# Performance work log

Measured on AMD Instinct MI355X. Metric: run time of the kernel, lower is better.

The kernel has to match this reference:

```python
import jax, jax.numpy as jnp
import numpy as np

B, LONG, SHORT, D, NH, HD = 512, 1000, 50, 64, 4, 16
NUM_ITEMS, TOPK = 100000, 50
NBUCKETS, HASHL, HASHD = 1024, 4, 16  # NOTE: 4 hash layers of D//4 so concat matches item_dim (source default 3 is a shape bug)


def lin(x, w, b):
    return x @ w.T + b


def ln(x, g, b):
    m = x.mean(-1, keepdims=True)
    v = ((x - m) ** 2).mean(-1, keepdims=True)
    return (x - m) / jnp.sqrt(v + 1e-5) * g + b


def setup_inputs() -> dict:
    key = jax.random.key(0)
    ks = jax.random.split(key, 24)
    rn = lambda i, s: jax.random.normal(ks[i], s, jnp.float32) * 0.02
    emb = rn(0, (NUM_ITEMS + 1, D)).at[0].set(0.0)  # padding_idx=0 row zeroed
    return dict(
        user_features=jax.random.normal(ks[1], (B, D), jnp.float32),
        target_item_id=jax.random.randint(ks[2], (B,), 0, NUM_ITEMS + 1),
        short_hist_ids=jax.random.randint(ks[3], (B, SHORT), 0, NUM_ITEMS + 1),
        long_hist_ids=jax.random.randint(ks[4], (B, LONG), 0, NUM_ITEMS + 1),
        item_emb=emb,
        tproj_w=rn(5, (D, D)), tproj_b=jnp.zeros((D,), jnp.float32),
        attn_w1=rn(6, (64, 3 * D)), attn_b1=jnp.zeros((64,), jnp.float32),
        attn_w2=rn(7, (1, 64)), attn_b2=jnp.zeros((1,), jnp.float32),
        hash_emb=rn(8, (HASHL, NBUCKETS, HASHD)),
        sdim_w=rn(9, (D, D)), sdim_b=jnp.zeros((D,), jnp.float32),
        tf_qkv_w=rn(10, (2, 3 * D, D)), tf_qkv_b=jnp.zeros((2, 3 * D), jnp.float32),
        tf_out_w=rn(11, (2, D, D)), tf_out_b=jnp.zeros((2, D), jnp.float32),
        tf_ln1_g=jnp.ones((2, D), jnp.float32), tf_ln1_b=jnp.zeros((2, D), jnp.float32),
        tf_ff1_w=rn(12, (2, 2 * D, D)), tf_ff1_b=jnp.zeros((2, 2 * D), jnp.float32),
        tf_ff2_w=rn(13, (2, D, 2 * D)), tf_ff2_b=jnp.zeros((2, D), jnp.float32),
        tf_ln2_g=jnp.ones((2, D), jnp.float32), tf_ln2_b=jnp.zeros((2, D), jnp.float32),
        fus_w1=rn(14, (256, 4 * D)), fus_b1=jnp.zeros((256,), jnp.float32),
        fus_w2=rn(15, (128, 256)), fus_b2=jnp.zeros((128,), jnp.float32),
        fus_w3=rn(16, (1, 128)), fus_b3=jnp.zeros((1,), jnp.float32),
    )


def sim_forward(user_features, item_emb, tproj_w, tproj_b, attn_w1, attn_b1,
                attn_w2, attn_b2, hash_emb, sdim_w, sdim_b, tf_qkv_w, tf_qkv_b,
                tf_out_w, tf_out_b, tf_ln1_g, tf_ln1_b, tf_ff1_w, tf_ff1_b,
                tf_ff2_w, tf_ff2_b, tf_ln2_g, tf_ln2_b, fus_w1, fus_b1, fus_w2,
                fus_b2, fus_w3, fus_b3, target_item_id, short_hist_ids, long_hist_ids):
    # target projection
    target_emb = lin(item_emb[target_item_id], tproj_w, tproj_b)         # [B,D]
    # ---- hard search over long history ----
    long_emb = item_emb[long_hist_ids]                                    # [B,L,D]
    t = jnp.broadcast_to(target_emb[:, None, :], long_emb.shape)
    cc = jnp.concatenate([t, long_emb, long_emb * t], axis=-1)            # [B,L,3D]
    scores = lin(jax.nn.relu(lin(cc, attn_w1, attn_b1)), attn_w2, attn_b2)[..., 0]
    attn = jax.nn.softmax(scores, axis=-1)                                # [B,L]
    top_w, top_i = jax.lax.top_k(attn, TOPK)
    top_w = jax.nn.softmax(top_w, axis=-1)
    top_e = jnp.take_along_axis(long_emb, top_i[..., None], axis=1)       # [B,K,D]
    hard_repr = (top_w[..., None] * top_e).sum(axis=1)                    # [B,D]
    # ---- SDIM soft search ----
    bucket = long_hist_ids % NBUCKETS
    h = hash_emb[:, bucket].mean(axis=2)                                  # [HL,B,HD]
    hash_repr = jnp.moveaxis(h, 0, 1).reshape(h.shape[1], HASHL * HASHD)  # [B,D]
    soft_repr = lin(hash_repr + long_emb.mean(axis=1), sdim_w, sdim_b)    # [B,D]
    # ---- BST transformer over short history (post-norm, relu, dropout=eval) ----
    x = item_emb[short_hist_ids]                                          # [B,S,D]
    for l in range(2):
        qkv = lin(x, tf_qkv_w[l], tf_qkv_b[l])
        q, k, v = jnp.split(qkv, 3, axis=-1)
        q = q.reshape(B, SHORT, NH, HD); k = k.reshape(B, SHORT, NH, HD); v = v.reshape(B, SHORT, NH, HD)
        sc = jnp.einsum('bqhd,bkhd->bhqk', q, k) / np.sqrt(HD).astype(np.float32)
        a = jax.nn.softmax(sc, axis=-1)
        o = jnp.einsum('bhqk,bkhd->bqhd', a, v).reshape(B, SHORT, D)
        x = ln(x + lin(o, tf_out_w[l], tf_out_b[l]), tf_ln1_g[l], tf_ln1_b[l])
        f = lin(jax.nn.relu(lin(x, tf_ff1_w[l], tf_ff1_b[l])), tf_ff2_w[l], tf_ff2_b[l])
        x = ln(x + f, tf_ln2_g[l], tf_ln2_b[l])
    bst_repr = x.mean(axis=1)                                             # [B,D]
    # ---- fusion MLP ----
    combined = jnp.concatenate([user_features, hard_repr, soft_repr, bst_repr], axis=-1)
    hdn = jax.nn.relu(lin(combined, fus_w1, fus_b1))
    hdn = jax.nn.relu(lin(hdn, fus_w2, fus_b2))
    return lin(hdn, fus_w3, fus_b3)[..., 0]                               # [B]


def reference(user_features, target_item_id, short_hist_ids, long_hist_ids,
              item_emb, tproj_w, tproj_b, attn_w1, attn_b1, attn_w2, attn_b2,
              hash_emb, sdim_w, sdim_b, tf_qkv_w, tf_qkv_b, tf_out_w, tf_out_b,
              tf_ln1_g, tf_ln1_b, tf_ff1_w, tf_ff1_b, tf_ff2_w, tf_ff2_b,
              tf_ln2_g, tf_ln2_b, fus_w1, fus_b1, fus_w2, fus_b2, fus_w3, fus_b3):
    return sim_forward(user_features, item_emb, tproj_w, tproj_b, attn_w1, attn_b1,
                       attn_w2, attn_b2, hash_emb, sdim_w, sdim_b, tf_qkv_w, tf_qkv_b,
                       tf_out_w, tf_out_b, tf_ln1_g, tf_ln1_b, tf_ff1_w, tf_ff1_b,
                       tf_ff2_w, tf_ff2_b, tf_ln2_g, tf_ln2_b, fus_w1, fus_b1,
                       fus_w2, fus_b2, fus_w3, fus_b3, target_item_id,
                       short_hist_ids, long_hist_ids)
```

## Files before the change

### kernel.cpp

```cpp
#include <hip/hip_runtime.h>
#include <math.h>

#define NB 512
#define LONGN 1000
#define SHORTN 50
#define TOPKN 50
#define HALFN 500
#define NG 8
#define EROW 72
#define BROW 72
#define F1ROW 136

typedef __attribute__((ext_vector_type(8))) short bf16x8;
typedef __attribute__((ext_vector_type(4))) float f32x4;

__device__ __forceinline__ float dot4(float4 a, float4 b) {
  return a.x*b.x + a.y*b.y + a.z*b.z + a.w*b.w;
}

template<int N>
__device__ __forceinline__ float dotN(const float* w, const float* x) {
  const float4* w4 = (const float4*)w;
  const float4* x4 = (const float4*)x;
  float a0 = 0.f, a1 = 0.f, a2 = 0.f, a3 = 0.f;
  #pragma unroll
  for (int k = 0; k < N/4; k += 4) {
    a0 += dot4(w4[k],   x4[k]);
    a1 += dot4(w4[k+1], x4[k+1]);
    a2 += dot4(w4[k+2], x4[k+2]);
    a3 += dot4(w4[k+3], x4[k+3]);
  }
  return (a0 + a1) + (a2 + a3);
}

__device__ __forceinline__ float wave_sum(float v) {
  #pragma unroll
  for (int off = 32; off > 0; off >>= 1) v += __shfl_xor(v, off);
  return v;
}
__device__ __forceinline__ float wave_max(float v) {
  #pragma unroll
  for (int off = 32; off > 0; off >>= 1) v = fmaxf(v, __shfl_xor(v, off));
  return v;
}

__device__ __forceinline__ unsigned short f2bf(float x) {
  unsigned u = __float_as_uint(x);
  return (unsigned short)((u + 0x7fffu + ((u >> 16) & 1u)) >> 16);
}

__global__ __launch_bounds__(256, 4) void hard_scores_kernel(
    const int* __restrict__ target_item_id,
    const int* __restrict__ long_hist_ids,
    const float* __restrict__ item_emb,
    const float* __restrict__ tproj_w, const float* __restrict__ tproj_b,
    const float* __restrict__ attn_w1, const float* __restrict__ attn_b1,
    const float* __restrict__ attn_w2, const float* __restrict__ attn_b2,
    const float* __restrict__ hash_emb,
    float* __restrict__ scores_ws, float* __restrict__ partA,
    float* __restrict__ partH)
{
  __shared__ __align__(16) short Abf[64*EROW];
  __shared__ __align__(16) short Ebuf[2][64*EROW];
  __shared__ __align__(16) float tv[64];
  __shared__ __align__(16) float te[64];
  __shared__ __align__(16) float2 cw[64];
  __shared__ int idsL[HALFN];
  __shared__ __align__(16) float redE[4*64];

  const int bid = blockIdx.x;
  const int b = bid >> 1, half = bid & 1;
  const int base = half * HALFN;
  const int tid = threadIdx.x;
  const int wid = tid >> 6, lane = tid & 63;

  if (tid < 64) tv[tid] = item_emb[target_item_id[b]*64 + tid];
  for (int l = tid; l < HALFN; l += 256) idsL[l] = long_hist_ids[b*LONGN + base + l];
  __syncthreads();
  if (tid < 64) te[tid] = tproj_b[tid] + dotN<64>(tproj_w + tid*64, tv);
  __syncthreads();
  if (tid < 64) {
    float c = attn_b1[tid] + dotN<64>(attn_w1 + tid*192, te);
    cw[tid] = make_float2(c, attn_w2[tid]);
  }
  for (int idx = tid; idx < 4096; idx += 256) {
    int i = idx >> 6, j = idx & 63;
    Abf[i*EROW + j] = (short)f2bf(attn_w1[i*192 + 64 + j] + attn_w1[i*192 + 128 + j]*te[j]);
  }
  __syncthreads();

  bf16x8 a00,a01,a10,a11,a20,a21,a30,a31;
  {
    const short* ap = Abf + (lane & 15)*EROW + ((lane >> 4) << 3);
    a00 = *(const bf16x8*)(ap +  0*EROW);  a01 = *(const bf16x8*)(ap +  0*EROW + 32);
    a10 = *(const bf16x8*)(ap + 16*EROW);  a11 = *(const bf16x8*)(ap + 16*EROW + 32);
    a20 = *(const bf16x8*)(ap + 32*EROW);  a21 = *(const bf16x8*)(ap + 32*EROW + 32);
    a30 = *(const bf16x8*)(ap + 48*EROW);  a31 = *(const bf16x8*)(ap + 48*EROW + 32);
  }

  const float b2s = attn_b2[0];
  const int it_g = tid >> 2;
  const int dimg = (tid & 3) * 16;

  float4 sE0 = {0,0,0,0}, sE1 = {0,0,0,0}, sE2 = {0,0,0,0}, sE3 = {0,0,0,0};

  {
    const float4* ep = (const float4*)(item_emb + (size_t)idsL[it_g]*64 + dimg);
    float4 r0 = ep[0], r1 = ep[1], r2 = ep[2], r3 = ep[3];
    sE0.x+=r0.x; sE0.y+=r0.y; sE0.z+=r0.z; sE0.w+=r0.w;
    sE1.x+=r1.x; sE1.y+=r1.y; sE1.z+=r1.z; sE1.w+=r1.w;
    sE2.x+=r2.x; sE2.y+=r2.y; sE2.z+=r2.z; sE2.w+=r2.w;
    sE3.x+=r3.x; sE3.y+=r3.y; sE3.z+=r3.z; sE3.w+=r3.w;
    bf16x8 w0, w1;
    w0[0]=(short)f2bf(r0.x); w0[1]=(short)f2bf(r0.y); w0[2]=(short)f2bf(r0.z); w0[3]=(short)f2bf(r0.w);
    w0[4]=(short)f2bf(r1.x); w0[5]=(short)f2bf(r1.y); w0[6]=(short)f2bf(r1.z); w0[7]=(short)f2bf(r1.w);
    w1[0]=(short)f2bf(r2.x); w1[1]=(short)f2bf(r2.y); w1[2]=(short)f2bf(r2.z); w1[3]=(short)f2bf(r2.w);
    w1[4]=(short)f2bf(r3.x); w1[5]=(short)f2bf(r3.y); w1[6]=(short)f2bf(r3.z); w1[7]=(short)f2bf(r3.w);
    short* dst = &Ebuf[0][it_g*EROW + dimg];
    *(bf16x8*)dst = w0;  *(bf16x8*)(dst + 8) = w1;
  }
  __syncthreads();

  int buf = 0;
  for (int g = 0; g < NG; ++g) {
    float4 r0={0,0,0,0}, r1={0,0,0,0}, r2={0,0,0,0}, r3={0,0,0,0};
    const bool more = (g + 1 < NG);
    if (more) {
      const int gi = (g+1)*64 + it_g;
      if (gi < HALFN) {
        const float4* ep = (const float4*)(item_emb + (size_t)idsL[gi]*64 + dimg);
        r0 = ep[0]; r1 = ep[1]; r2 = ep[2]; r3 = ep[3];
      }
    }

    f32x4 acc0={0,0,0,0}, acc1={0,0,0,0}, acc2={0,0,0,0}, acc3={0,0,0,0};
    {
      const short* ep = &Ebuf[buf][(wid*16 + (lane & 15))*EROW + ((lane >> 4) << 3)];
      bf16x8 b0 = *(const bf16x8*)(ep);
      bf16x8 b1 = *(const bf16x8*)(ep + 32);
      acc0 = __builtin_amdgcn_mfma_f32_16x16x32_bf16(a00, b0, acc0, 0, 0, 0);
      acc0 = __builtin_amdgcn_mfma_f32_16x16x32_bf16(a01, b1, acc0, 0, 0, 0);
      acc1 = __builtin_amdgcn_mfma_f32_16x16x32_bf16(a10, b0, acc1, 0, 0, 0);
      acc1 = __builtin_amdgcn_mfma_f32_16x16x32_bf16(a11, b1, acc1, 0, 0, 0);
      acc2 = __builtin_amdgcn_mfma_f32_16x16x32_bf16(a20, b0, acc2, 0, 0, 0);
      acc2 = __builtin_amdgcn_mfma_f32_16x16x32_bf16(a21, b1, acc2, 0, 0, 0);
      acc3 = __builtin_amdgcn_mfma_f32_16x16x32_bf16(a30, b0, acc3, 0, 0, 0);
      acc3 = __builtin_amdgcn_mfma_f32_16x16x32_bf16(a31, b1, acc3, 0, 0, 0);
    }
    float p = 0.f;
    {
      const int rbase = (lane >> 4) << 2;
      #pragma unroll
      for (int r = 0; r < 4; ++r) {
        float2 c0 = cw[ 0 + rbase + r];
        float2 c1 = cw[16 + rbase + r];
        float2 c2 = cw[32 + rbase + r];
        float2 c3 = cw[48 + rbase + r];
        p += c0.y * fmaxf(acc0[r] + c0.x, 0.f);
        p += c1.y * fmaxf(acc1[r] + c1.x, 0.f);
        p += c2.y * fmaxf(acc2[r] + c2.x, 0.f);
        p += c3.y * fmaxf(acc3[r] + c3.x, 0.f);
      }
    }
    p += __shfl_xor(p, 16);
    p += __shfl_xor(p, 32);
    if (lane < 16) {
      const int gi = g*64 + wid*16 + lane;
      if (gi < HALFN) scores_ws[b*LONGN + base + gi] = b2s + p;
    }

    if (more) {
      sE0.x+=r0.x; sE0.y+=r0.y; sE0.z+=r0.z; sE0.w+=r0.w;
      sE1.x+=r1.x; sE1.y+=r1.y; sE1.z+=r1.z; sE1.w+=r1.w;
      sE2.x+=r2.x; sE2.y+=r2.y; sE2.z+=r2.z; sE2.w+=r2.w;
      sE3.x+=r3.x; sE3.y+=r3.y; sE3.z+=r3.z; sE3.w+=r3.w;
      bf16x8 w0, w1;
      w0[0]=(short)f2bf(r0.x); w0[1]=(short)f2bf(r0.y); w0[2]=(short)f2bf(r0.z); w0[3]=(short)f2bf(r0.w);
      w0[4]=(short)f2bf(r1.x); w0[5]=(short)f2bf(r1.y); w0[6]=(short)f2bf(r1.z); w0[7]=(short)f2bf(r1.w);
      w1[0]=(short)f2bf(r2.x); w1[1]=(short)f2bf(r2.y); w1[2]=(short)f2bf(r2.z); w1[3]=(short)f2bf(r2.w);
      w1[4]=(short)f2bf(r3.x); w1[5]=(short)f2bf(r3.y); w1[6]=(short)f2bf(r3.z); w1[7]=(short)f2bf(r3.w);
      short* dst = &Ebuf[buf ^ 1][it_g*EROW + dimg];
      *(bf16x8*)dst = w0;  *(bf16x8*)(dst + 8) = w1;
    }
    __syncthreads();
    buf ^= 1;
  }

  {
    float* red = (float*)&Ebuf[0][0];
    const int b17 = tid * 17;
    red[b17+ 0]=sE0.x; red[b17+ 1]=sE0.y; red[b17+ 2]=sE0.z; red[b17+ 3]=sE0.w;
    red[b17+ 4]=sE1.x; red[b17+ 5]=sE1.y; red[b17+ 6]=sE1.z; red[b17+ 7]=sE1.w;
    red[b17+ 8]=sE2.x; red[b17+ 9]=sE2.y; red[b17+10]=sE2.z; red[b17+11]=sE2.w;
    red[b17+12]=sE3.x; red[b17+13]=sE3.y; red[b17+14]=sE3.z; red[b17+15]=sE3.w;
    __syncthreads();
    if (tid < 64) {
      const int dg = tid >> 4, dw = tid & 15;
      float s = 0.f;
      for (int j = 0; j < 64; ++j) s += red[(j*4 + dg)*17 + dw];
      partA[bid*64 + tid] = s;
    }
  }

  {
    const int hl = lane >> 4, dd = lane & 15;
    const float* hb = hash_emb + hl*1024*16 + dd;
    float accH = 0.f;
    for (int l = wid; l < HALFN; l += 4)
      accH += hb[(idsL[l] & 1023)*16];
    redE[wid*64 + lane] = accH;
  }
  __syncthreads();
  if (wid == 0)
    partH[bid*64 + lane] = redE[lane] + redE[64+lane] + redE[128+lane] + redE[192+lane];
}

__global__ __launch_bounds__(256) void bst_prep_kernel(
    const float* __restrict__ qkv_w, const float* __restrict__ out_w,
    const float* __restrict__ ff1_w, const float* __restrict__ ff2_w,
    short* __restrict__ wF)
{
  const int t = blockIdx.x*256 + threadIdx.x;
  if (t >= 8192) return;
  const int fid = t >> 6, lane = t & 63;
  const int n16 = lane & 15, k8 = (lane >> 4) * 8;
  const float* src;
  if (fid < 48)      { int f=fid,    l=f/24, r=f%24, nt=r>>1, kc=r&1;
    src = qkv_w + l*12288 + (nt*16+n16)*64 + kc*32 + k8; }
  else if (fid < 64) { int f=fid-48, l=f>>3, r=f&7,  nt=r>>1, kc=r&1;
    src = out_w + l*4096 + (nt*16+n16)*64 + kc*32 + k8; }
  else if (fid < 96) { int f=fid-64, l=f>>4, r=f&15, nt=r>>1, kc=r&1;
    src = ff1_w + l*8192 + (nt*16+n16)*64 + kc*32 + k8; }
  else               { int f=fid-96, l=f>>4, r=f&15, nt=r>>2, kc=r&3;
    src = ff2_w + l*8192 + (nt*16+n16)*128 + kc*32 + k8; }
  short* dst = wF + fid*512 + lane*8;
  #pragma unroll
  for (int j = 0; j < 8; ++j) dst[j] = (short)f2bf(src[j]);
}

__global__ __launch_bounds__(512, 2) void bst_kernel(
    const int* __restrict__ short_ids, const float* __restrict__ item_emb,
    const short* __restrict__ wF,
    const float* __restrict__ qkv_b, const float* __restrict__ out_b,
    const float* __restrict__ ln1_g, const float* __restrict__ ln1_b,
    const float* __restrict__ ff1_b, const float* __restrict__ ff2_b,
    const float* __restrict__ ln2_g, const float* __restrict__ ln2_b,
    float* __restrict__ bst_out)
{
  __shared__ __align__(16) float xf[SHORTN*64];
  __shared__ __align__(16) short xbf[64*BROW];
  __shared__ __align__(16) float qf[SHORTN*68];
  __shared__ __align__(16) float arena[SHORTN*132];
  __shared__ __align__(16) short obf[64*BROW];

  short* f1bf = (short*)arena;

  const int b = blockIdx.x, tid = threadIdx.x;
  const int w8 = tid >> 6, lane = tid & 63;
  const int mh = w8 & 1, wg = w8 >> 1;
  const int n16 = lane & 15;
  const int kg8 = (lane >> 4) << 3;
  const int mrow = (lane >> 4) << 2;
  const int rb = 32*mh;

  for (int idx = tid; idx < SHORTN*64; idx += 512) {
    int s = idx >> 6, j = idx & 63;
    float v = item_emb[short_ids[b*SHORTN + s]*64 + j];
    xf[idx] = v;
    xbf[s*BROW + j] = (short)f2bf(v);
  }
  for (int idx = tid; idx < 14*BROW; idx += 512) {
    xbf[50*BROW + idx] = 0;
    obf[50*BROW + idx] = 0;
  }
  __syncthreads();

  for (int l = 0; l < 2; ++l) {
    {
      const short* ap = xbf + (rb + n16)*BROW + kg8;
      bf16x8 A00 = *(const bf16x8*)(ap);            bf16x8 A01 = *(const bf16x8*)(ap + 32);
      bf16x8 A10 = *(const bf16x8*)(ap + 16*BROW);  bf16x8 A11 = *(const bf16x8*)(ap + 16*BROW + 32);
      #pragma unroll
      for (int t = 0; t < 3; ++t) {
        const int nt = wg*3 + t;
        const short* bp = wF + (size_t)(l*24 + nt*2)*512 + lane*8;
        bf16x8 B0 = *(const bf16x8*)(bp);
        bf16x8 B1 = *(const bf16x8*)(bp + 512);
        f32x4 c0={0,0,0,0}, c1={0,0,0,0};
        c0 = __builtin_amdgcn_mfma_f32_16x16x32_bf16(A00, B0, c0, 0,0,0);
        c0 = __builtin_amdgcn_mfma_f32_16x16x32_bf16(A01, B1, c0, 0,0,0);
        c1 = __builtin_amdgcn_mfma_f32_16x16x32_bf16(A10, B0, c1, 0,0,0);
        c1 = __builtin_amdgcn_mfma_f32_16x16x32_bf16(A11, B1, c1, 0,0,0);
        const int c = nt*16 + n16;
        const float bias = qkv_b[l*192 + c];
        #pragma unroll
        for (int r = 0; r < 4; ++r) {
          const int r0 = rb + mrow + r;
          const int r1 = r0 + 16;
          float v0 = c0[r] + bias;
          float v1 = c1[r] + bias;
          if (c < 64) {
            qf[r0*68 + c] = v0;
            if (r1 < SHORTN) qf[r1*68 + c] = v1;
          } else {
            const int cc = c - 64;
            arena[r0*132 + cc] = v0;
            if (r1 < SHORTN) arena[r1*132 + cc] = v1;
          }
        }
      }
    }
    __syncthreads();

    if (tid < 8*SHORTN) {
      const int pair = tid >> 1, khalf = tid & 1;
      const int h = pair / SHORTN, s = pair - h*SHORTN;
      const float4* qp = (const float4*)(qf + s*68 + h*16);
      const float4 qA = qp[0], qB2 = qp[1], qC = qp[2], qD = qp[3];
      float ss = 0.f;
      float4 oa0 = {0,0,0,0}, oa1 = {0,0,0,0}, oa2 = {0,0,0,0}, oa3 = {0,0,0,0};
      const int t0 = khalf*25;
      for (int t2 = t0; t2 < t0 + 25; ++t2) {
        const float4* kp = (const float4*)(arena + t2*132 + h*16);
        float d = dot4(qA,kp[0]) + dot4(qB2,kp[1]) + dot4(qC,kp[2]) + dot4(qD,kp[3]);
        float p = __expf(d*0.25f);
        ss += p;
        const float4* vp = (const float4*)(arena + t2*132 + 64 + h*16);
        float4 v0 = vp[0], v1 = vp[1], v2 = vp[2], v3 = vp[3];
        oa0.x += p*v0.x; oa0.y += p*v0.y; oa0.z += p*v0.z; oa0.w += p*v0.w;
        oa1.x += p*v1.x; oa1.y += p*v1.y; oa1.z += p*v1.z; oa1.w += p*v1.w;
        oa2.x += p*v2.x; oa2.y += p*v2.y; oa2.z += p*v2.z; oa2.w += p*v2.w;
        oa3.x += p*v3.x; oa3.y += p*v3.y; oa3.z += p*v3.z; oa3.w += p*v3.w;
      }
      ss    += __shfl_xor(ss, 1);
      oa0.x += __shfl_xor(oa0.x, 1); oa0.y += __shfl_xor(oa0.y, 1);
      oa0.z += __shfl_xor(oa0.z, 1); oa0.w += __shfl_xor(oa0.w, 1);
      oa1.x += __shfl_xor(oa1.x, 1); oa1.y += __shfl_xor(oa1.y, 1);
      oa1.z += __shfl_xor(oa1.z, 1); oa1.w += __shfl_xor(oa1.w, 1);
      oa2.x += __shfl_xor(oa2.x, 1); oa2.y += __shfl_xor(oa2.y, 1);
      oa2.z += __shfl_xor(oa2.z, 1); oa2.w += __shfl_xor(oa2.w, 1);
      oa3.x += __shfl_xor(oa3.x, 1); oa3.y += __shfl_xor(oa3.y, 1);
      oa3.z += __shfl_xor(oa3.z, 1); oa3.w += __shfl_xor(oa3.w, 1);
      if (khalf == 0) {
        const float inv = 1.f/ss;
        bf16x8 w0, w1;
        w0[0]=(short)f2bf(oa0.x*inv); w0[1]=(short)f2bf(oa0.y*inv);
        w0[2]=(short)f2bf(oa0.z*inv); w0[3]=(short)f2bf(oa0.w*inv);
        w0[4]=(short)f2bf(oa1.x*inv); w0[5]=(short)f2bf(oa1.y*inv);
        w0[6]=(short)f2bf(oa1.z*inv); w0[7]=(short)f2bf(oa1.w*inv);
        w1[0]=(short)f2bf(oa2.x*inv); w1[1]=(short)f2bf(oa2.y*inv);
        w1[2]=(short)f2bf(oa2.z*inv); w1[3]=(short)f2bf(oa2.w*inv);
        w1[4]=(short)f2bf(oa3.x*inv); w1[5]=(short)f2bf(oa3.y*inv);
        w1[6]=(short)f2bf(oa3.z*inv); w1[7]=(short)f2bf(oa3.w*inv);
        short* op = obf + s*BROW + h*16;
        *(bf16x8*)op = w0;  *(bf16x8*)(op + 8) = w1;
      }
    }
    __syncthreads();

    {
      const short* ap = obf + (rb + n16)*BROW + kg8;
      bf16x8 A00 = *(const bf16x8*)(ap);            bf16x8 A01 = *(const bf16x8*)(ap + 32);
      bf16x8 A10 = *(const bf16x8*)(ap + 16*BROW);  bf16x8 A11 = *(const bf16x8*)(ap + 16*BROW + 32);
      const int nt = wg;
      const short* bp = wF + (size_t)(48 + l*8 + nt*2)*512 + lane*8;
      bf16x8 B0 = *(const bf16x8*)(bp);
      bf16x8 B1 = *(const bf16x8*)(bp + 512);
      f32x4 c0={0,0,0,0}, c1={0,0,0,0};
      c0 = __builtin_amdgcn_mfma_f32_16x16x32_bf16(A00, B0, c0, 0,0,0);
      c0 = __builtin_amdgcn_mfma_f32_16x16x32_bf16(A01, B1, c0, 0,0,0);
      c1 = __builtin_amdgcn_mfma_f32_16x16x32_bf16(A10, B0, c1, 0,0,0);
      c1 = __builtin_amdgcn_mfma_f32_16x16x32_bf16(A11, B1, c1, 0,0,0);
      const int c = nt*16 + n16;
      const float bias = out_b[l*64 + c];
      #pragma unroll
      for (int r = 0; r < 4; ++r) {
        const int r0 = rb + mrow + r;
        const int r1 = r0 + 16;
        arena[r0*68 + c] = xf[r0*64 + c] + bias + c0[r];
        if (r1 < SHORTN) arena[r1*68 + c] = xf[r1*64 + c] + bias + c1[r];
      }
      for (int idx = tid; idx < 14*F1ROW; idx += 512) f1bf[50*F1ROW + idx] = 0;
    }
    __syncthreads();

    {
      const float g = ln1_g[l*64 + lane], bb = ln1_b[l*64 + lane];
      for (int s = w8; s < SHORTN; s += 8) {
        float y = arena[s*68 + lane];
        float mean = wave_sum(y) * (1.f/64.f);
        float dv = y - mean;
        float var = wave_sum(dv*dv) * (1.f/64.f);
        float r = dv / sqrtf(var + 1e-5f) * g + bb;
        xf[s*64 + lane] = r;
        xbf[s*BROW + lane] = (short)f2bf(r);
      }
    }
    __syncthreads();

    {
      const short* ap = xbf + (rb + n16)*BROW + kg8;
      bf16x8 A00 = *(const bf16x8*)(ap);            bf16x8 A01 = *(const bf16x8*)(ap + 32);
      bf16x8 A10 = *(const bf16x8*)(ap + 16*BROW);  bf16x8 A11 = *(const bf16x8*)(ap + 16*BROW + 32);
      #pragma unroll
      for (int t = 0; t < 2; ++t) {
        const int nt = wg*2 + t;
        const short* bp = wF + (size_t)(64 + l*16 + nt*2)*512 + lane*8;
        bf16x8 B0 = *(const bf16x8*)(bp);
        bf16x8 B1 = *(const bf16x8*)(bp + 512);
        f32x4 c0={0,0,0,0}, c1={0,0,0,0};
        c0 = __builtin_amdgcn_mfma_f32_16x16x32_bf16(A00, B0, c0, 0,0,0);
        c0 = __builtin_amdgcn_mfma_f32_16x16x32_bf16(A01, B1, c0, 0,0,0);
        c1 = __builtin_amdgcn_mfma_f32_16x16x32_bf16(A10, B0, c1, 0,0,0);
        c1 = __builtin_amdgcn_mfma_f32_16x16x32_bf16(A11, B1, c1, 0,0,0);
        const int c = nt*16 + n16;
        const float bias = ff1_b[l*128 + c];
        #pragma unroll
        for (int r = 0; r < 4; ++r) {
          const int r0 = rb + mrow + r;
          const int r1 = r0 + 16;
          f1bf[r0*F1ROW + c] = (short)f2bf(fmaxf(c0[r] + bias, 0.f));
          if (r1 < SHORTN) f1bf[r1*F1ROW + c] = (short)f2bf(fmaxf(c1[r] + bias, 0.f));
        }
      }
    }
    __syncthreads();

    {
      const int nt = wg;
      f32x4 c0={0,0,0,0}, c1={0,0,0,0};
      #pragma unroll
      for (int kc = 0; kc < 4; ++kc) {
        const short* ap = f1bf + (rb + n16)*F1ROW + kc*32 + kg8;
        bf16x8 A0 = *(const bf16x8*)(ap);
        bf16x8 A1 = *(const bf16x8*)(ap + 16*F1ROW);
        const short* bp = wF + (size_t)(96 + l*16 + nt*4 + kc)*512 + lane*8;
        bf16x8 B = *(const bf16x8*)(bp);
        c0 = __builtin_amdgcn_mfma_f32_16x16x32_bf16(A0, B, c0, 0,0,0);
        c1 = __builtin_amdgcn_mfma_f32_16x16x32_bf16(A1, B, c1, 0,0,0);
      }
      __syncthreads();
      const int c = nt*16 + n16;
      const float bias = ff2_b[l*64 + c];
      #pragma unroll
      for (int r = 0; r < 4; ++r) {
        const int r0 = rb + mrow + r;
        const int r1 = r0 + 16;
        arena[r0*68 + c] = xf[r0*64 + c] + bias + c0[r];
        if (r1 < SHORTN) arena[r1*68 + c] = xf[r1*64 + c] + bias + c1[r];
      }
    }
    __syncthreads();

    {
      const float g = ln2_g[l*64 + lane], bb = ln2_b[l*64 + lane];
      for (int s = w8; s < SHORTN; s += 8) {
        float y = arena[s*68 + lane];
        float mean = wave_sum(y) * (1.f/64.f);
        float dv = y - mean;
        float var = wave_sum(dv*dv) * (1.f/64.f);
        float r = dv / sqrtf(var + 1e-5f) * g + bb;
        xf[s*64 + lane] = r;
        xbf[s*BROW + lane] = (short)f2bf(r);
      }
    }
    __syncthreads();
  }

  float acc = 0.f;
  for (int s = w8; s < SHORTN; s += 8) acc += xf[s*64 + lane];
  qf[w8*64 + lane] = acc;
  __syncthreads();
  if (w8 == 0) {
    float t = qf[lane];
    #pragma unroll
    for (int w = 1; w < 8; ++w) t += qf[w*64 + lane];
    bst_out[b*64 + lane] = t * (1.f/50.f);
  }
}

__global__ __launch_bounds__(512) void hard_finish_fusion_kernel(
    const int* __restrict__ long_hist_ids,
    const float* __restrict__ item_emb,
    const float* __restrict__ sdim_w, const float* __restrict__ sdim_b,
    const float* __restrict__ scores_ws,
    const float* __restrict__ partA, const float* __restrict__ partH,
    const float* __restrict__ user, const float* __restrict__ bst,
    const float* __restrict__ w1, const float* __restrict__ b1,
    const float* __restrict__ w2, const float* __restrict__ b2,
    const float* __restrict__ w3, const float* __restrict__ b3,
    float* __restrict__ out)
{
  __shared__ __align__(16) float scores[LONGN];
  __shared__ int   idsL[LONGN];
  __shared__ __align__(16) unsigned long long kv[1024];
  __shared__ __align__(16) float redE[8*64];
  __shared__ __align__(16) float vecbuf[64];
  __shared__ float redV[8];
  __shared__ float selV[TOPKN];
  __shared__ int   selI[TOPKN];
  __shared__ __align__(16) float comb[256];
  __shared__ __align__(16) float h1[256];
  __shared__ __align__(16) float h2[128];

  const int b = blockIdx.x;
  const int tid = threadIdx.x;
  const int wid = tid >> 6, lane = tid & 63;

  for (int l = tid; l < LONGN; l += 512) {
    scores[l] = scores_ws[b*LONGN + l];
    idsL[l] = long_hist_ids[b*LONGN + l];
  }
  if (tid < 64)                          comb[tid] = user[b*64 + tid];
  else if (tid >= 192 && tid < 256)      comb[tid] = bst[b*64 + tid - 192];
  __syncthreads();

  if (tid < 64)
    vecbuf[tid] = (partA[(2*b)*64 + tid] + partA[(2*b+1)*64 + tid]
                 + partH[(2*b)*64 + tid] + partH[(2*b+1)*64 + tid]) * (1.f/1000.f);
  __syncthreads();
  if (tid < 64)
    comb[128 + tid] = sdim_b[tid] + dotN<64>(sdim_w + tid*64, vecbuf);

  float mx = -INFINITY;
  for (int l = tid; l < LONGN; l += 512) mx = fmaxf(mx, scores[l]);
  mx = wave_max(mx);
  if (lane == 0) redV[wid] = mx;
  __syncthreads();
  mx = redV[0];
  #pragma unroll
  for (int w = 1; w < 8; ++w) mx = fmaxf(mx, redV[w]);
  __syncthreads();
  float sm = 0.f;
  for (int l = tid; l < LONGN; l += 512) {
    float a = expf(scores[l] - mx);
    scores[l] = a;
    sm += a;
  }
  sm = wave_sum(sm);
  if (lane == 0) redV[wid] = sm;
  __syncthreads();
  {
    float tot = redV[0];
    #pragma unroll
    for (int w = 1; w < 8; ++w) tot += redV[w];
    const float inv = 1.f / tot;
    for (int l = tid; l < LONGN; l += 512) scores[l] *= inv;
  }
  __syncthreads();

  for (int l = tid; l < 1024; l += 512) {
    if (l < LONGN) {
      unsigned vb = __float_as_uint(scores[l]);
      kv[l] = ((unsigned long long)(~vb) << 32) | (unsigned)l;
    } else {
      kv[l] = 0xFFFFFFFFFFFFFFFFull;
    }
  }
  __syncthreads();

  for (int k = 2; k <= 1024; k <<= 1) {
    for (int j = k >> 1; j > 0; j >>= 1) {
      {
        const int p = tid;
        const int i = ((p & ~(j-1)) << 1) | (p & (j-1));
        const int m = i + j;
        const bool up = ((i & k) == 0);
        unsigned long long a = kv[i], c = kv[m];
        if ((a > c) == up) { kv[i] = c; kv[m] = a; }
      }
      __syncthreads();
    }
  }

  if (tid < TOPKN) {
    unsigned long long key = kv[tid];
    selI[tid] = (int)(unsigned)(key & 0xFFFFFFFFu);
    selV[tid] = __uint_as_float(~(unsigned)(key >> 32));
  }
  __syncthreads();

  if (wid == 0) {
    float v = (lane < TOPKN) ? selV[lane] : -INFINITY;
    float m2 = wave_max(v);
    float e = (lane < TOPKN) ? expf(v - m2) : 0.f;
    float s2 = wave_sum(e);
    if (lane < TOPKN) selV[lane] = e / s2;
  }
  __syncthreads();

  float accR = 0.f;
  for (int r = wid; r < TOPKN; r += 8)
    accR += selV[r] * item_emb[idsL[selI[r]]*64 + lane];
  redE[wid*64 + lane] = accR;
  __syncthreads();
  if (wid == 0) {
    float t = redE[lane];
    #pragma unroll
    for (int w = 1; w < 8; ++w) t += redE[w*64 + lane];
    comb[64 + lane] = t;
  }
  __syncthreads();

  if (tid < 256) h1[tid] = fmaxf(b1[tid] + dotN<256>(w1 + tid*256, comb), 0.f);
  __syncthreads();
  if (tid < 128) h2[tid] = fmaxf(b2[tid] + dotN<256>(w2 + tid*256, h1), 0.f);
  __syncthreads();
  if (tid < 64) {
    float p = w3[tid]*h2[tid] + w3[tid+64]*h2[tid+64];
    p = wave_sum(p);
    if (tid == 0) out[b] = p + b3[0];
  }
}

extern "C" void kernel_launch(void* const* d_in, const int* in_sizes, int n_in,
                              void* d_out, int out_size, void* d_ws, size_t ws_size,
                              hipStream_t stream) {
  const float* user_features  = (const float*)d_in[0];
  const int*   target_item_id = (const int*)  d_in[1];
  const int*   short_hist_ids = (const int*)  d_in[2];
  const int*   long_hist_ids  = (const int*)  d_in[3];
  const float* item_emb       = (const float*)d_in[4];
  const float* tproj_w  = (const float*)d_in[5];
  const float* tproj_b  = (const float*)d_in[6];
  const float* attn_w1  = (const float*)d_in[7];
  const float* attn_b1  = (const float*)d_in[8];
  const float* attn_w2  = (const float*)d_in[9];
  const float* attn_b2  = (const float*)d_in[10];
  const float* hash_emb = (const float*)d_in[11];
  const float* sdim_w   = (const float*)d_in[12];
  const float* sdim_b   = (const float*)d_in[13];
  const float* tf_qkv_w = (const float*)d_in[14];
  const float* tf_qkv_b = (const float*)d_in[15];
  const float* tf_out_w = (const float*)d_in[16];
  const float* tf_out_b = (const float*)d_in[17];
  const float* tf_ln1_g = (const float*)d_in[18];
  const float* tf_ln1_b = (const float*)d_in[19];
  const float* tf_ff1_w = (const float*)d_in[20];
  const float* tf_ff1_b = (const float*)d_in[21];
  const float* tf_ff2_w = (const float*)d_in[22];
  const float* tf_ff2_b = (const float*)d_in[23];
  const float* tf_ln2_g = (const float*)d_in[24];
  const float* tf_ln2_b = (const float*)d_in[25];
  const float* fus_w1   = (const float*)d_in[26];
  const float* fus_b1   = (const float*)d_in[27];
  const float* fus_w2   = (const float*)d_in[28];
  const float* fus_b2   = (const float*)d_in[29];
  const float* fus_w3   = (const float*)d_in[30];
  const float* fus_b3   = (const float*)d_in[31];

  float* ws = (float*)d_ws;
  float* hard = ws;
  float* soft = hard + NB*64;
  float* bst  = soft + NB*64;
  float* scores_ws = bst + NB*64;
  float* partA = scores_ws + NB*LONGN;
  float* partH = partA + NB*2*64;
  short* wF    = (short*)(partH + NB*2*64);

  bst_prep_kernel<<<32, 256, 0, stream>>>(tf_qkv_w, tf_out_w, tf_ff1_w, tf_ff2_w, wF);
  hard_scores_kernel<<<2*NB, 256, 0, stream>>>(target_item_id, long_hist_ids,
      item_emb, tproj_w, tproj_b, attn_w1, attn_b1, attn_w2, attn_b2,
      hash_emb, scores_ws, partA, partH);
  bst_kernel<<<NB, 512, 0, stream>>>(short_hist_ids, item_emb, wF,
      tf_qkv_b, tf_out_b, tf_ln1_g, tf_ln1_b, tf_ff1_b, tf_ff2_b,
      tf_ln2_g, tf_ln2_b, bst);
  hard_finish_fusion_kernel<<<NB, 512, 0, stream>>>(long_hist_ids, item_emb,
      sdim_w, sdim_b, scores_ws, partA, partH,
      user_features, bst, fus_w1, fus_b1, fus_w2, fus_b2, fus_w3, fus_b3,
      (float*)d_out);
}
```

Before: 141.5 us.

## Fold BST weight prep into hard_scores and deepen gather prefetch to two groups

```diff
diff --git a/kernel.cpp b/kernel.cpp
--- a/kernel.cpp
+++ b/kernel.cpp
@@ -49,7 +49,7 @@
   return (unsigned short)((u + 0x7fffu + ((u >> 16) & 1u)) >> 16);
 }
 
-__global__ __launch_bounds__(256, 4) void hard_scores_kernel(
+__global__ __launch_bounds__(256, 3) void hard_scores_kernel(
     const int* __restrict__ target_item_id,
     const int* __restrict__ long_hist_ids,
     const float* __restrict__ item_emb,
@@ -57,6 +57,9 @@
     const float* __restrict__ attn_w1, const float* __restrict__ attn_b1,
     const float* __restrict__ attn_w2, const float* __restrict__ attn_b2,
     const float* __restrict__ hash_emb,
+    const float* __restrict__ qkv_w, const float* __restrict__ out_w,
+    const float* __restrict__ ff1_w, const float* __restrict__ ff2_w,
+    short* __restrict__ wF,
     float* __restrict__ scores_ws, float* __restrict__ partA,
     float* __restrict__ partH)
 {
@@ -74,6 +77,24 @@
   const int tid = threadIdx.x;
   const int wid = tid >> 6, lane = tid & 63;
 
+  if (bid < 32) {
+    const int t = bid*256 + tid;
+    const int fid = t >> 6, plane = t & 63;
+    const int n16p = plane & 15, k8 = (plane >> 4) * 8;
+    const float* src;
+    if (fid < 48)      { int f=fid,    l=f/24, r=f%24, nt=r>>1, kc=r&1;
+      src = qkv_w + l*12288 + (nt*16+n16p)*64 + kc*32 + k8; }
+    else if (fid < 64) { int f=fid-48, l=f>>3, r=f&7,  nt=r>>1, kc=r&1;
+      src = out_w + l*4096 + (nt*16+n16p)*64 + kc*32 + k8; }
+    else if (fid < 96) { int f=fid-64, l=f>>4, r=f&15, nt=r>>1, kc=r&1;
+      src = ff1_w + l*8192 + (nt*16+n16p)*64 + kc*32 + k8; }
+    else               { int f=fid-96, l=f>>4, r=f&15, nt=r>>2, kc=r&3;
+      src = ff2_w + l*8192 + (nt*16+n16p)*128 + kc*32 + k8; }
+    short* dst = wF + fid*512 + plane*8;
+    #pragma unroll
+    for (int j = 0; j < 8; ++j) dst[j] = (short)f2bf(src[j]);
+  }
+
   if (tid < 64) tv[tid] = item_emb[target_item_id[b]*64 + tid];
   for (int l = tid; l < HALFN; l += 256) idsL[l] = long_hist_ids[b*LONGN + base + l];
   __syncthreads();
@@ -103,88 +124,90 @@
   const int dimg = (tid & 3) * 16;
 
   float4 sE0 = {0,0,0,0}, sE1 = {0,0,0,0}, sE2 = {0,0,0,0}, sE3 = {0,0,0,0};
-
-  {
-    const float4* ep = (const float4*)(item_emb + (size_t)idsL[it_g]*64 + dimg);
-    float4 r0 = ep[0], r1 = ep[1], r2 = ep[2], r3 = ep[3];
-    sE0.x+=r0.x; sE0.y+=r0.y; sE0.z+=r0.z; sE0.w+=r0.w;
-    sE1.x+=r1.x; sE1.y+=r1.y; sE1.z+=r1.z; sE1.w+=r1.w;
-    sE2.x+=r2.x; sE2.y+=r2.y; sE2.z+=r2.z; sE2.w+=r2.w;
-    sE3.x+=r3.x; sE3.y+=r3.y; sE3.z+=r3.z; sE3.w+=r3.w;
-    bf16x8 w0, w1;
-    w0[0]=(short)f2bf(r0.x); w0[1]=(short)f2bf(r0.y); w0[2]=(short)f2bf(r0.z); w0[3]=(short)f2bf(r0.w);
-    w0[4]=(short)f2bf(r1.x); w0[5]=(short)f2bf(r1.y); w0[6]=(short)f2bf(r1.z); w0[7]=(short)f2bf(r1.w);
-    w1[0]=(short)f2bf(r2.x); w1[1]=(short)f2bf(r2.y); w1[2]=(short)f2bf(r2.z); w1[3]=(short)f2bf(r2.w);
-    w1[4]=(short)f2bf(r3.x); w1[5]=(short)f2bf(r3.y); w1[6]=(short)f2bf(r3.z); w1[7]=(short)f2bf(r3.w);
-    short* dst = &Ebuf[0][it_g*EROW + dimg];
-    *(bf16x8*)dst = w0;  *(bf16x8*)(dst + 8) = w1;
-  }
-  __syncthreads();
-
-  int buf = 0;
-  for (int g = 0; g < NG; ++g) {
-    float4 r0={0,0,0,0}, r1={0,0,0,0}, r2={0,0,0,0}, r3={0,0,0,0};
-    const bool more = (g + 1 < NG);
-    if (more) {
-      const int gi = (g+1)*64 + it_g;
-      if (gi < HALFN) {
-        const float4* ep = (const float4*)(item_emb + (size_t)idsL[gi]*64 + dimg);
-        r0 = ep[0]; r1 = ep[1]; r2 = ep[2]; r3 = ep[3];
-      }
-    }
-
-    f32x4 acc0={0,0,0,0}, acc1={0,0,0,0}, acc2={0,0,0,0}, acc3={0,0,0,0};
-    {
-      const short* ep = &Ebuf[buf][(wid*16 + (lane & 15))*EROW + ((lane >> 4) << 3)];
-      bf16x8 b0 = *(const bf16x8*)(ep);
-      bf16x8 b1 = *(const bf16x8*)(ep + 32);
-      acc0 = __builtin_amdgcn_mfma_f32_16x16x32_bf16(a00, b0, acc0, 0, 0, 0);
-      acc0 = __builtin_amdgcn_mfma_f32_16x16x32_bf16(a01, b1, acc0, 0, 0, 0);
-      acc1 = __builtin_amdgcn_mfma_f32_16x16x32_bf16(a10, b0, acc1, 0, 0, 0);
-      acc1 = __builtin_amdgcn_mfma_f32_16x16x32_bf16(a11, b1, acc1, 0, 0, 0);
-      acc2 = __builtin_amdgcn_mfma_f32_16x16x32_bf16(a20, b0, acc2, 0, 0, 0);
-      acc2 = __builtin_amdgcn_mfma_f32_16x16x32_bf16(a21, b1, acc2, 0, 0, 0);
-      acc3 = __builtin_amdgcn_mfma_f32_16x16x32_bf16(a30, b0, acc3, 0, 0, 0);
-      acc3 = __builtin_amdgcn_mfma_f32_16x16x32_bf16(a31, b1, acc3, 0, 0, 0);
-    }
-    float p = 0.f;
-    {
-      const int rbase = (lane >> 4) << 2;
-      #pragma unroll
-      for (int r = 0; r < 4; ++r) {
-        float2 c0 = cw[ 0 + rbase + r];
-        float2 c1 = cw[16 + rbase + r];
-        float2 c2 = cw[32 + rbase + r];
-        float2 c3 = cw[48 + rbase + r];
-        p += c0.y * fmaxf(acc0[r] + c0.x, 0.f);
-        p += c1.y * fmaxf(acc1[r] + c1.x, 0.f);
-        p += c2.y * fmaxf(acc2[r] + c2.x, 0.f);
-        p += c3.y * fmaxf(acc3[r] + c3.x, 0.f);
-      }
-    }
-    p += __shfl_xor(p, 16);
-    p += __shfl_xor(p, 32);
-    if (lane < 16) {
-      const int gi = g*64 + wid*16 + lane;
-      if (gi < HALFN) scores_ws[b*LONGN + base + gi] = b2s + p;
-    }
-
-    if (more) {
-      sE0.x+=r0.x; sE0.y+=r0.y; sE0.z+=r0.z; sE0.w+=r0.w;
-      sE1.x+=r1.x; sE1.y+=r1.y; sE1.z+=r1.z; sE1.w+=r1.w;
-      sE2.x+=r2.x; sE2.y+=r2.y; sE2.z+=r2.z; sE2.w+=r2.w;
-      sE3.x+=r3.x; sE3.y+=r3.y; sE3.z+=r3.z; sE3.w+=r3.w;
-      bf16x8 w0, w1;
-      w0[0]=(short)f2bf(r0.x); w0[1]=(short)f2bf(r0.y); w0[2]=(short)f2bf(r0.z); w0[3]=(short)f2bf(r0.w);
-      w0[4]=(short)f2bf(r1.x); w0[5]=(short)f2bf(r1.y); w0[6]=(short)f2bf(r1.z); w0[7]=(short)f2bf(r1.w);
-      w1[0]=(short)f2bf(r2.x); w1[1]=(short)f2bf(r2.y); w1[2]=(short)f2bf(r2.z); w1[3]=(short)f2bf(r2.w);
-      w1[4]=(short)f2bf(r3.x); w1[5]=(short)f2bf(r3.y); w1[6]=(short)f2bf(r3.z); w1[7]=(short)f2bf(r3.w);
-      short* dst = &Ebuf[buf ^ 1][it_g*EROW + dimg];
-      *(bf16x8*)dst = w0;  *(bf16x8*)(dst + 8) = w1;
-    }
-    __syncthreads();
-    buf ^= 1;
-  }
+  float4 pA0, pA1, pA2, pA3;
+  float4 pB0, pB1, pB2, pB3;
+
+#define LOADG(G, R0, R1, R2, R3)                                              \
+  {                                                                           \
+    R0 = make_float4(0,0,0,0); R1 = R0; R2 = R0; R3 = R0;                     \
+    const int gi_ = (G)*64 + it_g;                                            \
+    if (gi_ < HALFN) {                                                        \
+      const float4* ep_ = (const float4*)(item_emb + (size_t)idsL[gi_]*64 + dimg); \
+      R0 = ep_[0]; R1 = ep_[1]; R2 = ep_[2]; R3 = ep_[3];                     \
+    }                                                                         \
+  }
+
+#define STOREG(DST, R0, R1, R2, R3)                                           \
+  {                                                                           \
+    sE0.x+=R0.x; sE0.y+=R0.y; sE0.z+=R0.z; sE0.w+=R0.w;                       \
+    sE1.x+=R1.x; sE1.y+=R1.y; sE1.z+=R1.z; sE1.w+=R1.w;                       \
+    sE2.x+=R2.x; sE2.y+=R2.y; sE2.z+=R2.z; sE2.w+=R2.w;                       \
+    sE3.x+=R3.x; sE3.y+=R3.y; sE3.z+=R3.z; sE3.w+=R3.w;                       \
+    bf16x8 w0_, w1_;                                                          \
+    w0_[0]=(short)f2bf(R0.x); w0_[1]=(short)f2bf(R0.y);                       \
+    w0_[2]=(short)f2bf(R0.z); w0_[3]=(short)f2bf(R0.w);                       \
+    w0_[4]=(short)f2bf(R1.x); w0_[5]=(short)f2bf(R1.y);                       \
+    w0_[6]=(short)f2bf(R1.z); w0_[7]=(short)f2bf(R1.w);                       \
+    w1_[0]=(short)f2bf(R2.x); w1_[1]=(short)f2bf(R2.y);                       \
+    w1_[2]=(short)f2bf(R2.z); w1_[3]=(short)f2bf(R2.w);                       \
+    w1_[4]=(short)f2bf(R3.x); w1_[5]=(short)f2bf(R3.y);                       \
+    w1_[6]=(short)f2bf(R3.z); w1_[7]=(short)f2bf(R3.w);                       \
+    short* dst_ = &Ebuf[DST][it_g*EROW + dimg];                               \
+    *(bf16x8*)dst_ = w0_;  *(bf16x8*)(dst_ + 8) = w1_;                        \
+  }
+
+#define COMPUTEG(BUF, G)                                                      \
+  {                                                                           \
+    f32x4 acc0={0,0,0,0}, acc1={0,0,0,0}, acc2={0,0,0,0}, acc3={0,0,0,0};     \
+    const short* ep_ = &Ebuf[BUF][(wid*16 + (lane & 15))*EROW + ((lane >> 4) << 3)]; \
+    bf16x8 b0_ = *(const bf16x8*)(ep_);                                       \
+    bf16x8 b1_ = *(const bf16x8*)(ep_ + 32);                                  \
+    acc0 = __builtin_amdgcn_mfma_f32_16x16x32_bf16(a00, b0_, acc0, 0,0,0);    \
+    acc0 = __builtin_amdgcn_mfma_f32_16x16x32_bf16(a01, b1_, acc0, 0,0,0);    \
+    acc1 = __builtin_amdgcn_mfma_f32_16x16x32_bf16(a10, b0_, acc1, 0,0,0);    \
+    acc1 = __builtin_amdgcn_mfma_f32_16x16x32_bf16(a11, b1_, acc1, 0,0,0);    \
+    acc2 = __builtin_amdgcn_mfma_f32_16x16x32_bf16(a20, b0_, acc2, 0,0,0);    \
+    acc2 = __builtin_amdgcn_mfma_f32_16x16x32_bf16(a21, b1_, acc2, 0,0,0);    \
+    acc3 = __builtin_amdgcn_mfma_f32_16x16x32_bf16(a30, b0_, acc3, 0,0,0);    \
+    acc3 = __builtin_amdgcn_mfma_f32_16x16x32_bf16(a31, b1_, acc3, 0,0,0);    \
+    float p_ = 0.f;                                                           \
+    const int rbase_ = (lane >> 4) << 2;                                      \
+    _Pragma("unroll")                                                         \
+    for (int r = 0; r < 4; ++r) {                                             \
+      float2 c0_ = cw[ 0 + rbase_ + r];                                       \
+      float2 c1_ = cw[16 + rbase_ + r];                                       \
+      float2 c2_ = cw[32 + rbase_ + r];                                       \
+      float2 c3_ = cw[48 + rbase_ + r];                                       \
+      p_ += c0_.y * fmaxf(acc0[r] + c0_.x, 0.f);                              \
+      p_ += c1_.y * fmaxf(acc1[r] + c1_.x, 0.f);                              \
+      p_ += c2_.y * fmaxf(acc2[r] + c2_.x, 0.f);                              \
+      p_ += c3_.y * fmaxf(acc3[r] + c3_.x, 0.f);                              \
+    }                                                                         \
+    p_ += __shfl_xor(p_, 16);                                                 \
+    p_ += __shfl_xor(p_, 32);                                                 \
+    if (lane < 16) {                                                          \
+      const int gi_ = (G)*64 + wid*16 + lane;                                 \
+      if (gi_ < HALFN) scores_ws[b*LONGN + base + gi_] = b2s + p_;            \
+    }                                                                         \
+  }
+
+  LOADG(0, pA0, pA1, pA2, pA3);
+  LOADG(1, pB0, pB1, pB2, pB3);
+  STOREG(0, pA0, pA1, pA2, pA3);
+  __syncthreads();
+
+  LOADG(2, pA0, pA1, pA2, pA3);  COMPUTEG(0, 0);  STOREG(1, pB0, pB1, pB2, pB3);  __syncthreads();
+  LOADG(3, pB0, pB1, pB2, pB3);  COMPUTEG(1, 1);  STOREG(0, pA0, pA1, pA2, pA3);  __syncthreads();
+  LOADG(4, pA0, pA1, pA2, pA3);  COMPUTEG(0, 2);  STOREG(1, pB0, pB1, pB2, pB3);  __syncthreads();
+  LOADG(5, pB0, pB1, pB2, pB3);  COMPUTEG(1, 3);  STOREG(0, pA0, pA1, pA2, pA3);  __syncthreads();
+  LOADG(6, pA0, pA1, pA2, pA3);  COMPUTEG(0, 4);  STOREG(1, pB0, pB1, pB2, pB3);  __syncthreads();
+  LOADG(7, pB0, pB1, pB2, pB3);  COMPUTEG(1, 5);  STOREG(0, pA0, pA1, pA2, pA3);  __syncthreads();
+                                 COMPUTEG(0, 6);  STOREG(1, pB0, pB1, pB2, pB3);  __syncthreads();
+                                 COMPUTEG(1, 7);
+
+#undef LOADG
+#undef STOREG
+#undef COMPUTEG
 
   {
     float* red = (float*)&Ebuf[0][0];
@@ -213,29 +236,6 @@
   __syncthreads();
   if (wid == 0)
     partH[bid*64 + lane] = redE[lane] + redE[64+lane] + redE[128+lane] + redE[192+lane];
-}
-
-__global__ __launch_bounds__(256) void bst_prep_kernel(
-    const float* __restrict__ qkv_w, const float* __restrict__ out_w,
-    const float* __restrict__ ff1_w, const float* __restrict__ ff2_w,
-    short* __restrict__ wF)
-{
-  const int t = blockIdx.x*256 + threadIdx.x;
-  if (t >= 8192) return;
-  const int fid = t >> 6, lane = t & 63;
-  const int n16 = lane & 15, k8 = (lane >> 4) * 8;
-  const float* src;
-  if (fid < 48)      { int f=fid,    l=f/24, r=f%24, nt=r>>1, kc=r&1;
-    src = qkv_w + l*12288 + (nt*16+n16)*64 + kc*32 + k8; }
-  else if (fid < 64) { int f=fid-48, l=f>>3, r=f&7,  nt=r>>1, kc=r&1;
-    src = out_w + l*4096 + (nt*16+n16)*64 + kc*32 + k8; }
-  else if (fid < 96) { int f=fid-64, l=f>>4, r=f&15, nt=r>>1, kc=r&1;
-    src = ff1_w + l*8192 + (nt*16+n16)*64 + kc*32 + k8; }
-  else               { int f=fid-96, l=f>>4, r=f&15, nt=r>>2, kc=r&3;
-    src = ff2_w + l*8192 + (nt*16+n16)*128 + kc*32 + k8; }
-  short* dst = wF + fid*512 + lane*8;
-  #pragma unroll
-  for (int j = 0; j < 8; ++j) dst[j] = (short)f2bf(src[j]);
 }
 
 __global__ __launch_bounds__(512, 2) void bst_kernel(
@@ -658,10 +658,10 @@
   float* partH = partA + NB*2*64;
   short* wF    = (short*)(partH + NB*2*64);
 
-  bst_prep_kernel<<<32, 256, 0, stream>>>(tf_qkv_w, tf_out_w, tf_ff1_w, tf_ff2_w, wF);
   hard_scores_kernel<<<2*NB, 256, 0, stream>>>(target_item_id, long_hist_ids,
       item_emb, tproj_w, tproj_b, attn_w1, attn_b1, attn_w2, attn_b2,
-      hash_emb, scores_ws, partA, partH);
+      hash_emb, tf_qkv_w, tf_out_w, tf_ff1_w, tf_ff2_w, wF,
+      scores_ws, partA, partH);
   bst_kernel<<<NB, 512, 0, stream>>>(short_hist_ids, item_emb, wF,
       tf_qkv_b, tf_out_b, tf_ln1_g, tf_ln1_b, tf_ff1_b, tf_ff2_b,
       tf_ln2_g, tf_ln2_b, bst);
```

New measurement: 185.1 us. +30.8%, slower.
